# Optimization experiments

Measured on AMD Instinct MI355X. Metric: run time of the kernel, lower is better.

The kernel has to match this reference:

```python
import jax, jax.numpy as jnp
import numpy as np

ALPHA = 0.25
GAMMA = 2.0
EPS = 1e-8
COST_CLASS_W = 1.0
COST_KP_W = 1.0


def setup_inputs() -> dict:
    key = jax.random.key(0)
    k1, k2, k3 = jax.random.split(key, 3)
    bs, nq, num_classes, T, D = 16, 1024, 2, 64, 63
    pred_logits = jax.random.normal(k1, (bs, nq, num_classes), dtype=jnp.float32)
    pred_keypoints = jax.random.normal(k2, (bs, nq, D), dtype=jnp.float32)
    tgt_kp = jax.random.normal(k3, (T, D), dtype=jnp.float32)  # ~half > 0 -> occlusion mask
    tgt_ids = jnp.ones((T,), dtype=jnp.int64)  # all 'hand' class; hand_idx all True
    return {"pred_logits": pred_logits, "pred_keypoints": pred_keypoints,
            "tgt_kp": tgt_kp, "tgt_ids": tgt_ids}


def reference(pred_logits, pred_keypoints, tgt_kp, tgt_ids):
    bs, nq, _ = pred_logits.shape
    out_prob = jax.nn.sigmoid(pred_logits.reshape(bs * nq, -1))   # [Q, C]
    out_kp = pred_keypoints.reshape(bs * nq, -1)                  # [Q, 63]

    # Focal-style classification cost
    neg = (1.0 - ALPHA) * out_prob ** GAMMA * (-jnp.log1p(-(out_prob - EPS) - 1.0 + 1.0) if False else -jnp.log(1.0 - out_prob + EPS))
    pos = ALPHA * (1.0 - out_prob) ** GAMMA * (-jnp.log(out_prob + EPS))
    cost_class = pos[:, tgt_ids] - neg[:, tgt_ids]                # [Q, T]

    # Masked L1 'cdist': only visible (tgt_kp > 0) coordinates contribute.
    occl_mask = (tgt_kp > 0).astype(out_kp.dtype)                 # [T, 63]
    diff = jnp.abs(out_kp[:, None, :] - tgt_kp[None, :, :])       # [Q, T, 63]
    cost_kp = jnp.sum(diff * occl_mask[None, :, :], axis=-1)      # [Q, T]

    C = COST_KP_W * cost_kp + COST_CLASS_W * cost_class
    return C.reshape(bs, nq, -1)  # [bs, nq, T]; CPU Hungarian (scipy) consumes per-sample blocks
```

## Files before the change

kernel.cpp:

```cpp
#include <hip/hip_runtime.h>


#define ALPHA 0.25f
#define EPS 1e-8f

constexpr int Q  = 16 * 1024;
constexpr int T  = 64;
constexpr int D  = 63;
constexpr int QB = 64;
constexpr int P  = 68;
constexpr int P4 = 17;

__device__ inline float focal_cost(float x) {
  float p   = 1.0f / (1.0f + __expf(-x));
  float pos = ALPHA * (1.0f - p) * (1.0f - p) * (-__logf(p + EPS));
  float neg = (1.0f - ALPHA) * p * p * (-__logf(1.0f - p + EPS));
  return pos - neg;
}

__device__ inline unsigned int to_bf16_rne(float v) {
  unsigned int x = __float_as_uint(v);
  return (x + 0x7FFFu + ((x >> 16) & 1u)) >> 16;
}

__global__ __launch_bounds__(256) void matcher_kernel(
    const float* __restrict__ logits,
    const float* __restrict__ kp,
    const float* __restrict__ tgt,
    const int*   __restrict__ ids,
    float* __restrict__ out)
{
  __shared__ __align__(16) float        As[64 * P];
  __shared__ __align__(16) unsigned int Bp[64 * P];
  __shared__ float Lcc[QB * 2];
  __shared__ int   Ids[T];

  const int tid   = threadIdx.x;
  const int qbase = blockIdx.x * QB;

  {
    const float4* src = (const float4*)(kp + qbase * D);
    for (int j = tid; j < QB * D / 4; j += 256) {
      float4 v = src[j];
      int i0 = 4 * j;
      float vv[4] = {v.x, v.y, v.z, v.w};
#pragma unroll
      for (int c = 0; c < 4; ++c) {
        int idx = i0 + c;
        int q = idx / D;
        int d = idx - q * D;
        As[d * P + q] = vv[c];
      }
    }
  }
  {
    const float4* src = (const float4*)tgt;
    for (int j = tid; j < T * D / 4; j += 256) {
      float4 v = src[j];
      int i0 = 4 * j;
      float vv[4] = {v.x, v.y, v.z, v.w};
#pragma unroll
      for (int c = 0; c < 4; ++c) {
        int idx = i0 + c;
        int t = idx / D;
        int d = idx - t * D;
        unsigned int bv = to_bf16_rne(vv[c]);
        unsigned int bm = (vv[c] > 0.0f) ? 0x3F80u : 0x0000u;
        Bp[d * P + t] = (bv << 16) | bm;
      }
    }
  }
  if (tid < QB * 2) Lcc[tid] = focal_cost(logits[qbase * 2 + tid]);
  if (tid < T) Ids[tid] = ids[tid];
  __syncthreads();

  const int qg = tid >> 4;
  const int tg = tid & 15;

  float4 acc0 = make_float4(0.f, 0.f, 0.f, 0.f);
  float4 acc1 = acc0, acc2 = acc0, acc3 = acc0;

  const float4* As4 = (const float4*)As;
  const uint4*  Bp4 = (const uint4*)Bp;

#pragma unroll 7
  for (int d = 0; d < D; ++d) {
    float4 a = As4[d * P4 + qg];
    uint4  w = Bp4[d * P4 + tg];
#define COL(acc_field, wf)                                   \
    {                                                        \
      float bv = __uint_as_float(wf & 0xFFFF0000u);          \
      float bm = __uint_as_float(wf << 16);                  \
      acc0.acc_field += bm * fabsf(a.x - bv);                \
      acc1.acc_field += bm * fabsf(a.y - bv);                \
      acc2.acc_field += bm * fabsf(a.z - bv);                \
      acc3.acc_field += bm * fabsf(a.w - bv);                \
    }
    COL(x, w.x)
    COL(y, w.y)
    COL(z, w.z)
    COL(w, w.w)
#undef COL
  }

  const int t0 = tg * 4;
  int id0 = min(max(Ids[t0 + 0], 0), 1);
  int id1 = min(max(Ids[t0 + 1], 0), 1);
  int id2 = min(max(Ids[t0 + 2], 0), 1);
  int id3 = min(max(Ids[t0 + 3], 0), 1);

  float4 accs[4] = {acc0, acc1, acc2, acc3};
#pragma unroll
  for (int i = 0; i < 4; ++i) {
    int ql = qg * 4 + i;
    float cc[2] = {Lcc[ql * 2 + 0], Lcc[ql * 2 + 1]};
    float4 r;
    r.x = accs[i].x + cc[id0];
    r.y = accs[i].y + cc[id1];
    r.z = accs[i].z + cc[id2];
    r.w = accs[i].w + cc[id3];
    *(float4*)&out[(qbase + ql) * T + t0] = r;
  }
}

extern "C" void kernel_launch(void* const* d_in, const int* in_sizes, int n_in,
                              void* d_out, int out_size, void* d_ws, size_t ws_size,
                              hipStream_t stream) {
  const float* logits = (const float*)d_in[0];
  const float* kp     = (const float*)d_in[1];
  const float* tgt    = (const float*)d_in[2];
  const int*   ids    = (const int*)d_in[3];
  float* out = (float*)d_out;

  matcher_kernel<<<dim3(Q / QB), dim3(256), 0, stream>>>(logits, kp, tgt, ids, out);
}
```

Before: 73.80 us.

## Read queries from global directly, keep fp32 targets, use 512-thread blocks

Stops staging the query keypoints in LDS: each thread now reads its four query rows straight from global memory, which are uniform across the 32 lanes of a group and so act as broadcast loads. Targets are kept as separate fp32 value and mask arrays instead of packed bf16 with a mask, which removes the bf16 rounding. The block grows to 512 threads, each computing a 4x2 tile instead of 4x4. This removes the transposed LDS writes for the queries but adds scalar global loads in the inner loop, halves the work per thread, and lowers arithmetic intensity.

After: 70.63 us. 1.04x faster.

```diff
diff --git a/kernel.cpp b/kernel.cpp
--- a/kernel.cpp
+++ b/kernel.cpp
@@ -9,7 +9,7 @@
 constexpr int D  = 63;
 constexpr int QB = 64;
 constexpr int P  = 68;
-constexpr int P4 = 17;
+constexpr int P2 = 34;
 
 __device__ inline float focal_cost(float x) {
   float p   = 1.0f / (1.0f + __expf(-x));
@@ -18,20 +18,15 @@
   return pos - neg;
 }
 
-__device__ inline unsigned int to_bf16_rne(float v) {
-  unsigned int x = __float_as_uint(v);
-  return (x + 0x7FFFu + ((x >> 16) & 1u)) >> 16;
-}
-
-__global__ __launch_bounds__(256) void matcher_kernel(
+__global__ __launch_bounds__(512) void matcher_kernel(
     const float* __restrict__ logits,
     const float* __restrict__ kp,
     const float* __restrict__ tgt,
     const int*   __restrict__ ids,
     float* __restrict__ out)
 {
-  __shared__ __align__(16) float        As[64 * P];
-  __shared__ __align__(16) unsigned int Bp[64 * P];
+  __shared__ __align__(16) float Bv[64 * P];
+  __shared__ __align__(16) float Bm[64 * P];
   __shared__ float Lcc[QB * 2];
   __shared__ int   Ids[T];
 
@@ -39,23 +34,8 @@
   const int qbase = blockIdx.x * QB;
 
   {
-    const float4* src = (const float4*)(kp + qbase * D);
-    for (int j = tid; j < QB * D / 4; j += 256) {
-      float4 v = src[j];
-      int i0 = 4 * j;
-      float vv[4] = {v.x, v.y, v.z, v.w};
-#pragma unroll
-      for (int c = 0; c < 4; ++c) {
-        int idx = i0 + c;
-        int q = idx / D;
-        int d = idx - q * D;
-        As[d * P + q] = vv[c];
-      }
-    }
-  }
-  {
     const float4* src = (const float4*)tgt;
-    for (int j = tid; j < T * D / 4; j += 256) {
+    for (int j = tid; j < T * D / 4; j += 512) {
       float4 v = src[j];
       int i0 = 4 * j;
       float vv[4] = {v.x, v.y, v.z, v.w};
@@ -64,9 +44,8 @@
         int idx = i0 + c;
         int t = idx / D;
         int d = idx - t * D;
-        unsigned int bv = to_bf16_rne(vv[c]);
-        unsigned int bm = (vv[c] > 0.0f) ? 0x3F80u : 0x0000u;
-        Bp[d * P + t] = (bv << 16) | bm;
+        Bv[d * P + t] = vv[c];
+        Bm[d * P + t] = (vv[c] > 0.0f) ? 1.0f : 0.0f;
       }
     }
   }
@@ -74,52 +53,48 @@
   if (tid < T) Ids[tid] = ids[tid];
   __syncthreads();
 
-  const int qg = tid >> 4;
-  const int tg = tid & 15;
+  const int qg = tid >> 5;
+  const int tg = tid & 31;
 
-  float4 acc0 = make_float4(0.f, 0.f, 0.f, 0.f);
-  float4 acc1 = acc0, acc2 = acc0, acc3 = acc0;
+  const float* __restrict__ r0 = kp + (qbase + qg * 4 + 0) * D;
+  const float* __restrict__ r1 = kp + (qbase + qg * 4 + 1) * D;
+  const float* __restrict__ r2 = kp + (qbase + qg * 4 + 2) * D;
+  const float* __restrict__ r3 = kp + (qbase + qg * 4 + 3) * D;
 
-  const float4* As4 = (const float4*)As;
-  const uint4*  Bp4 = (const uint4*)Bp;
+  float2 acc0 = make_float2(0.f, 0.f);
+  float2 acc1 = acc0, acc2 = acc0, acc3 = acc0;
+
+  const float2* Bv2 = (const float2*)Bv;
+  const float2* Bm2 = (const float2*)Bm;
 
 #pragma unroll 7
   for (int d = 0; d < D; ++d) {
-    float4 a = As4[d * P4 + qg];
-    uint4  w = Bp4[d * P4 + tg];
-#define COL(acc_field, wf)                                   \
-    {                                                        \
-      float bv = __uint_as_float(wf & 0xFFFF0000u);          \
-      float bm = __uint_as_float(wf << 16);                  \
-      acc0.acc_field += bm * fabsf(a.x - bv);                \
-      acc1.acc_field += bm * fabsf(a.y - bv);                \
-      acc2.acc_field += bm * fabsf(a.z - bv);                \
-      acc3.acc_field += bm * fabsf(a.w - bv);                \
-    }
-    COL(x, w.x)
-    COL(y, w.y)
-    COL(z, w.z)
-    COL(w, w.w)
-#undef COL
+    float a0 = r0[d], a1 = r1[d], a2 = r2[d], a3 = r3[d];
+    float2 bv = Bv2[d * P2 + tg];
+    float2 bm = Bm2[d * P2 + tg];
+    acc0.x += bm.x * fabsf(a0 - bv.x);
+    acc0.y += bm.y * fabsf(a0 - bv.y);
+    acc1.x += bm.x * fabsf(a1 - bv.x);
+    acc1.y += bm.y * fabsf(a1 - bv.y);
+    acc2.x += bm.x * fabsf(a2 - bv.x);
+    acc2.y += bm.y * fabsf(a2 - bv.y);
+    acc3.x += bm.x * fabsf(a3 - bv.x);
+    acc3.y += bm.y * fabsf(a3 - bv.y);
   }
 
-  const int t0 = tg * 4;
+  const int t0 = tg * 2;
   int id0 = min(max(Ids[t0 + 0], 0), 1);
   int id1 = min(max(Ids[t0 + 1], 0), 1);
-  int id2 = min(max(Ids[t0 + 2], 0), 1);
-  int id3 = min(max(Ids[t0 + 3], 0), 1);
 
-  float4 accs[4] = {acc0, acc1, acc2, acc3};
+  float2 accs[4] = {acc0, acc1, acc2, acc3};
 #pragma unroll
   for (int i = 0; i < 4; ++i) {
     int ql = qg * 4 + i;
     float cc[2] = {Lcc[ql * 2 + 0], Lcc[ql * 2 + 1]};
-    float4 r;
+    float2 r;
     r.x = accs[i].x + cc[id0];
     r.y = accs[i].y + cc[id1];
-    r.z = accs[i].z + cc[id2];
-    r.w = accs[i].w + cc[id3];
-    *(float4*)&out[(qbase + ql) * T + t0] = r;
+    *(float2*)&out[(qbase + ql) * T + t0] = r;
   }
 }
 
@@ -132,5 +107,5 @@
   const int*   ids    = (const int*)d_in[3];
   float* out = (float*)d_out;
 
-  matcher_kernel<<<dim3(Q / QB), dim3(256), 0, stream>>>(logits, kp, tgt, ids, out);
+  matcher_kernel<<<dim3(Q / QB), dim3(512), 0, stream>>>(logits, kp, tgt, ids, out);
 }
```
